# Kernel optimization log

Hardware: AMD Instinct MI355X
Metric: run time of the kernel (lower is better)

## Reference

```python
import jax, jax.numpy as jnp
import numpy as np

N_HEAD = 16
CHUNK_SIZE = 64
TOP_B = 8
LOCAL_WINDOW = 256


def _l2_normalize(x, eps=1e-12):
    # matches torch F.normalize(dim=-1): x / max(||x||, eps)
    n = jnp.sqrt(jnp.sum(x * x, axis=-1, keepdims=True))
    return x / jnp.maximum(n, eps)


def setup_inputs() -> dict:
    key = jax.random.key(0)
    ks = jax.random.split(key, 9)
    B, T, C = 2, 2048, 1024
    s = lambda fan_in: 1.0 / np.sqrt(fan_in)
    return {
        "x": jax.random.normal(ks[0], (B, T, C), jnp.float32),
        "Wqkv": jax.random.normal(ks[1], (C, 3 * C), jnp.float32) * s(C),
        "bqkv": jax.random.normal(ks[2], (3 * C,), jnp.float32) * 0.02,
        "Wproj": jax.random.normal(ks[3], (C, C), jnp.float32) * s(C),
        "bproj": jax.random.normal(ks[4], (C,), jnp.float32) * 0.02,
        "Wrouter": jax.random.normal(ks[5], (C, 32), jnp.float32) * s(C),
        "brouter": jax.random.normal(ks[6], (32,), jnp.float32) * 0.02,
        "Wq_rt": jax.random.normal(ks[7], (C, 32), jnp.float32) * s(C),
        "bq_rt": jax.random.normal(ks[8], (32,), jnp.float32) * 0.02,
    }


def reference(x, Wqkv, bqkv, Wproj, bproj, Wrouter, brouter, Wq_rt, bq_rt):
    B, T, C = x.shape
    H = N_HEAD
    D = C // H

    # --- qkv projection ---
    qkv = x @ Wqkv + bqkv                       # [B,T,3C]
    q, k, v = jnp.split(qkv, 3, axis=-1)
    q = q.reshape(B, T, H, D).transpose(0, 2, 1, 3)  # [B,H,T,D]
    k = k.reshape(B, T, H, D).transpose(0, 2, 1, 3)
    v = v.reshape(B, T, H, D).transpose(0, 2, 1, 3)

    # --- routing (T > local_window + chunk_size) ---
    num_chunks = T // CHUNK_SIZE                 # T divisible -> no padding, mask all-True
    chunk_means = x.reshape(B, num_chunks, CHUNK_SIZE, C).mean(axis=2)  # [B,N,C]
    routing_embeds = chunk_means @ Wrouter + brouter                     # [B,N,32]
    q_rt = _l2_normalize(x @ Wq_rt + bq_rt)                              # [B,T,32]
    re_n = _l2_normalize(routing_embeds)
    routing_scores = jnp.einsum('btd,bnd->btn', q_rt, re_n)              # [B,T,N]
    _, chunk_indices = jax.lax.top_k(routing_scores, TOP_B)              # [B,T,top_b]

    # --- dense causal attention (forward path uses is_causal SDPA) ---
    scale = 1.0 / jnp.sqrt(jnp.asarray(D, x.dtype))
    scores = jnp.einsum('bhqd,bhkd->bhqk', q, k) * scale                 # [B,H,T,T]
    causal = jnp.tril(jnp.ones((T, T), dtype=bool))
    scores = jnp.where(causal[None, None], scores, -jnp.inf)
    attn = jax.nn.softmax(scores, axis=-1)
    y = jnp.einsum('bhqk,bhkd->bhqd', attn, v)                           # [B,H,T,D]
    y = y.transpose(0, 2, 1, 3).reshape(B, T, C)
    y = y @ Wproj + bproj

    return y, chunk_indices, routing_scores, routing_embeds
```

## Files before the change

kernel.cpp:

```cpp
#include <hip/hip_runtime.h>
#include <hip/hip_bf16.h>
#include <math.h>

#define B_   2
#define T_   2048
#define C_   1024
#define H_   16
#define D_   64
#define NCH  32
#define RD   32
#define TOPB 8

typedef __attribute__((ext_vector_type(8))) short bf16x8;
typedef __attribute__((ext_vector_type(4))) float f32x4;

static __device__ __forceinline__ unsigned short f2b(float f) {
    return __bfloat16_as_ushort(__float2bfloat16(f));
}

__global__ __launch_bounds__(256) void cast_bf16_kernel(
    const float* __restrict__ in, unsigned short* __restrict__ out, int n8)
{
    const int i = blockIdx.x * blockDim.x + threadIdx.x;
    if (i >= n8) return;
    float4 a = ((const float4*)in)[i * 2];
    float4 b = ((const float4*)in)[i * 2 + 1];
    bf16x8 o;
    o[0] = (short)f2b(a.x); o[1] = (short)f2b(a.y);
    o[2] = (short)f2b(a.z); o[3] = (short)f2b(a.w);
    o[4] = (short)f2b(b.x); o[5] = (short)f2b(b.y);
    o[6] = (short)f2b(b.z); o[7] = (short)f2b(b.w);
    *(bf16x8*)&out[i * 8] = o;
}

__global__ __launch_bounds__(256) void transpose_cast_kernel(
    const float* __restrict__ W, unsigned short* __restrict__ Wt, int K, int N)
{
    __shared__ float t[64][65];
    const int tid = threadIdx.x;
    const int n0 = blockIdx.x * 64, k0 = blockIdx.y * 64;
#pragma unroll
    for (int i = 0; i < 4; i++) {
        const int f = tid + i * 256;
        const int r = f >> 4, c4 = (f & 15) * 4;
        float4 v = *(const float4*)&W[(size_t)(k0 + r) * N + n0 + c4];
        t[r][c4 + 0] = v.x; t[r][c4 + 1] = v.y;
        t[r][c4 + 2] = v.z; t[r][c4 + 3] = v.w;
    }
    __syncthreads();
#pragma unroll
    for (int i = 0; i < 2; i++) {
        const int s = tid + i * 256;
        const int rn = s >> 3, ck8 = (s & 7) * 8;
        bf16x8 o;
#pragma unroll
        for (int j = 0; j < 8; j++) o[j] = (short)f2b(t[ck8 + j][rn]);
        *(bf16x8*)&Wt[(size_t)(n0 + rn) * K + k0 + ck8] = o;
    }
}

template <int MODE>
__global__ __launch_bounds__(256) void gemm_mfma(
    const unsigned short* __restrict__ A, const unsigned short* __restrict__ Bt,
    const float* __restrict__ bias, float* __restrict__ out,
    unsigned short* __restrict__ qp, unsigned short* __restrict__ kp,
    unsigned short* __restrict__ vp, int M, int N, int K)
{
    __shared__ unsigned short As[2][128 * 32];
    __shared__ unsigned short Bs[2][128 * 32];

    const int tid  = threadIdx.x;
    const int lane = tid & 63;
    const int wave = tid >> 6;
    const int lr = lane & 15, lg = lane >> 4;
    const int wm = wave >> 1, wn = wave & 1;
    const int n0 = blockIdx.x * 128, m0 = blockIdx.y * 128;

    const int srow = tid >> 2;
    const int scol = (tid & 3) * 8;
    const unsigned short* ga = A  + (size_t)(m0 + srow) * K + scol;
    const unsigned short* gb = Bt + (size_t)(n0 + srow) * K + scol;
    const int ldst = (tid & 0xC0) * 8;

    f32x4 acc[4][4];
#pragma unroll
    for (int i = 0; i < 4; i++)
#pragma unroll
        for (int j = 0; j < 4; j++) acc[i][j] = (f32x4){0.f, 0.f, 0.f, 0.f};

#define GSTAGE(buf, k0)                                                        \
    _Pragma("unroll")                                                          \
    for (int i = 0; i < 2; i++) {                                              \
        __builtin_amdgcn_global_load_lds(                                      \
            (const __attribute__((address_space(1))) int*)(ga + (k0) + (size_t)i * 64 * K), \
            (__attribute__((address_space(3))) int*)&As[buf][i * 2048 + ldst], 16, 0, 0);   \
        __builtin_amdgcn_global_load_lds(                                      \
            (const __attribute__((address_space(1))) int*)(gb + (k0) + (size_t)i * 64 * K), \
            (__attribute__((address_space(3))) int*)&Bs[buf][i * 2048 + ldst], 16, 0, 0);   \
    }

    const int nt = K >> 5;
    GSTAGE(0, 0);
    __syncthreads();

    int cur = 0;
    for (int t = 0; t < nt; ++t) {
        if (t + 1 < nt) {
            GSTAGE(cur ^ 1, (t + 1) << 5);
        }

        bf16x8 af[4], bfr[4];
#pragma unroll
        for (int mi = 0; mi < 4; mi++)
            af[mi] = *(const bf16x8*)&As[cur][(wm * 64 + mi * 16 + lr) * 32 + lg * 8];
#pragma unroll
        for (int ni = 0; ni < 4; ni++)
            bfr[ni] = *(const bf16x8*)&Bs[cur][(wn * 64 + ni * 16 + lr) * 32 + lg * 8];
#pragma unroll
        for (int mi = 0; mi < 4; mi++)
#pragma unroll
            for (int ni = 0; ni < 4; ni++)
                acc[mi][ni] = __builtin_amdgcn_mfma_f32_16x16x32_bf16(
                    af[mi], bfr[ni], acc[mi][ni], 0, 0, 0);

        __syncthreads();
        cur ^= 1;
    }
#undef GSTAGE

#pragma unroll
    for (int ni = 0; ni < 4; ni++) {
        const int col = n0 + wn * 64 + ni * 16 + lr;
        const float bv = bias[col];
        if (MODE == 0) {
#pragma unroll
            for (int mi = 0; mi < 4; mi++) {
#pragma unroll
                for (int r = 0; r < 4; r++) {
                    const int row = m0 + wm * 64 + mi * 16 + lg * 4 + r;
                    out[(size_t)row * N + col] = acc[mi][ni][r] + bv;
                }
            }
        } else {
            const int which = col >> 10;
            const int c  = col & 1023;
            const int hh = c >> 6;
            const int dd = c & 63;
            unsigned short* dst = (which == 0) ? qp : (which == 1) ? kp : vp;
#pragma unroll
            for (int mi = 0; mi < 4; mi++) {
#pragma unroll
                for (int r = 0; r < 4; r++) {
                    const int row = m0 + wm * 64 + mi * 16 + lg * 4 + r;
                    const int bb = row >> 11, tt = row & 2047;
                    dst[(((size_t)bb * H_ + hh) * T_ + tt) * D_ + dd] =
                        f2b(acc[mi][ni][r] + bv);
                }
            }
        }
    }
}

__global__ void chunk_mean_kernel(const float* __restrict__ x, float* __restrict__ cm)
{
    const int bc = blockIdx.x;
    const int b = bc >> 5, n = bc & 31;
    const int c = blockIdx.y * 256 + threadIdx.x;
    const float* xp = x + ((size_t)b * T_ + n * 64) * C_;
    float s = 0.f;
    for (int i = 0; i < 64; i++) s += xp[(size_t)i * C_ + c];
    cm[(size_t)bc * C_ + c] = s * (1.0f / 64.0f);
}

__global__ void rowgemm32(const float* __restrict__ A, const float* __restrict__ W,
                          const float* __restrict__ bias, float* __restrict__ dst,
                          int M, int normalize)
{
    const int row  = blockIdx.x * 8 + (threadIdx.x >> 5);
    const int lane = threadIdx.x & 31;
    if (row >= M) return;
    const float* a = A + (size_t)row * C_;
    float acc = 0.f;
    for (int k = 0; k < C_; k += 4) {
        float4 a4 = *(const float4*)&a[k];
        acc += a4.x * W[(k + 0) * RD + lane];
        acc += a4.y * W[(k + 1) * RD + lane];
        acc += a4.z * W[(k + 2) * RD + lane];
        acc += a4.w * W[(k + 3) * RD + lane];
    }
    acc += bias[lane];
    if (normalize) {
        float ss = acc * acc;
#pragma unroll
        for (int off = 16; off >= 1; off >>= 1) ss += __shfl_xor(ss, off, 32);
        acc = acc / fmaxf(sqrtf(ss), 1e-12f);
    }
    dst[(size_t)row * RD + lane] = acc;
}

__global__ void l2norm_rows(const float* __restrict__ src, float* __restrict__ dst, int M)
{
    const int row  = blockIdx.x * 8 + (threadIdx.x >> 5);
    const int lane = threadIdx.x & 31;
    if (row >= M) return;
    float v = src[(size_t)row * RD + lane];
    float ss = v * v;
#pragma unroll
    for (int off = 16; off >= 1; off >>= 1) ss += __shfl_xor(ss, off, 32);
    dst[(size_t)row * RD + lane] = v / fmaxf(sqrtf(ss), 1e-12f);
}

__global__ __launch_bounds__(256) void qrt_kernel(
    const float* __restrict__ x, const float* __restrict__ W,
    const float* __restrict__ bias, float* __restrict__ dst)
{
    __shared__ float part[8][4][32];
    const int r0 = blockIdx.x * 4;
    const int g = threadIdx.x >> 5;
    const int n = threadIdx.x & 31;

    const float* w  = W + (size_t)(g * 128) * RD + n;
    const float* a0 = x + (size_t)(r0 + 0) * C_ + g * 128;
    const float* a1 = x + (size_t)(r0 + 1) * C_ + g * 128;
    const float* a2 = x + (size_t)(r0 + 2) * C_ + g * 128;
    const float* a3 = x + (size_t)(r0 + 3) * C_ + g * 128;

    float acc0 = 0.f, acc1 = 0.f, acc2 = 0.f, acc3 = 0.f;
#pragma unroll 8
    for (int i = 0; i < 128; i += 4) {
        const float w0 = w[(i + 0) * RD];
        const float w1 = w[(i + 1) * RD];
        const float w2 = w[(i + 2) * RD];
        const float w3 = w[(i + 3) * RD];
        float4 x0 = *(const float4*)&a0[i];
        float4 x1 = *(const float4*)&a1[i];
        float4 x2 = *(const float4*)&a2[i];
        float4 x3 = *(const float4*)&a3[i];
        acc0 += x0.x * w0; acc0 += x0.y * w1; acc0 += x0.z * w2; acc0 += x0.w * w3;
        acc1 += x1.x * w0; acc1 += x1.y * w1; acc1 += x1.z * w2; acc1 += x1.w * w3;
        acc2 += x2.x * w0; acc2 += x2.y * w1; acc2 += x2.z * w2; acc2 += x2.w * w3;
        acc3 += x3.x * w0; acc3 += x3.y * w1; acc3 += x3.z * w2; acc3 += x3.w * w3;
    }
    part[g][0][n] = acc0;
    part[g][1][n] = acc1;
    part[g][2][n] = acc2;
    part[g][3][n] = acc3;
    __syncthreads();

    if (g < 4) {
        float s = part[0][g][n];
#pragma unroll
        for (int gg = 1; gg < 8; gg++) s += part[gg][g][n];
        s += bias[n];
        float ss = s * s;
#pragma unroll
        for (int off = 16; off >= 1; off >>= 1) ss += __shfl_xor(ss, off, 32);
        dst[(size_t)(r0 + g) * RD + n] = s / fmaxf(sqrtf(ss), 1e-12f);
    }
}

__global__ void scores_topk(const float* __restrict__ qrt, const float* __restrict__ ren,
                            float* __restrict__ sc_out, float* __restrict__ idx_out)
{
    const int row = blockIdx.x * 64 + threadIdx.x;
    if (row >= B_ * T_) return;
    const int b = row / T_;
    float q[RD];
#pragma unroll
    for (int i = 0; i < RD; i++) q[i] = qrt[(size_t)row * RD + i];
    const float* rb = ren + (size_t)b * NCH * RD;
    float s[NCH];
#pragma unroll 4
    for (int n = 0; n < NCH; n++) {
        float acc = 0.f;
#pragma unroll
        for (int i = 0; i < RD; i++) acc += q[i] * rb[n * RD + i];
        s[n] = acc;
        sc_out[(size_t)row * NCH + n] = acc;
    }
    unsigned mask = 0;
    for (int t = 0; t < TOPB; t++) {
        float best = -INFINITY;
        int bi = 0;
#pragma unroll
        for (int n = 0; n < NCH; n++) {
            const bool ok = !((mask >> n) & 1u) && (s[n] > best);
            if (ok) { best = s[n]; bi = n; }
        }
        mask |= (1u << bi);
        idx_out[(size_t)row * TOPB + t] = (float)bi;
    }
}

#define LSTR 68
#define SCALE2 0.18033688f

__global__ __launch_bounds__(256) void attn_mfma(
    const unsigned short* __restrict__ qg, const unsigned short* __restrict__ kg,
    const unsigned short* __restrict__ vg, unsigned short* __restrict__ y)
{
    const int bid = blockIdx.x;
    const int xcd = bid & 7;
    const int j   = bid >> 3;
    const int h   = xcd + 8 * (j & 1);
    const int b   = (j >> 1) & 1;
    const int qt  = 31 - (j >> 2);

    const int tid  = threadIdx.x;
    const int wave = tid >> 6;
    const int lane = tid & 63;
    const int lg = lane >> 4;
    const int lr = lane & 15;

    __shared__ short Ks[2][64][LSTR];
    __shared__ short Vt[2][64][LSTR];

    const size_t base = ((size_t)(b * H_ + h) * T_) * D_;

    bf16x8 qf0, qf1;
    {
        const short* qp = (const short*)qg + base + (size_t)(qt * 64 + wave * 16 + lr) * D_;
        qf0 = *(const bf16x8*)&qp[lg * 8];
        qf1 = *(const bf16x8*)&qp[32 + lg * 8];
    }

    const int srr = tid >> 2;
    const int sc0 = (tid & 3) * 16;
    const int vrp = tid & 31;
    const int vcg = tid >> 5;
    const int kv0   = 2 * vrp;
    const int vslot = ((kv0 >> 5) << 5) + (((kv0 >> 2) & 3) << 3) +
                      (((kv0 >> 4) & 1) << 2) + (kv0 & 3);

    bf16x8 kreg0, kreg1, vreg0, vreg1;

    float m_run = -INFINITY, l_run = 0.f;
    f32x4 oacc[4];
#pragma unroll
    for (int r = 0; r < 4; r++) oacc[r] = (f32x4){0.f, 0.f, 0.f, 0.f};
    const int qrow_g = qt * 64 + wave * 16 + lr;

    {
        const short* kp = (const short*)kg + base + (size_t)srr * D_ + sc0;
        kreg0 = *(const bf16x8*)kp;
        kreg1 = *(const bf16x8*)(kp + 8);
        const short* vp = (const short*)vg + base + (size_t)kv0 * D_ + vcg * 8;
        vreg0 = *(const bf16x8*)vp;
        vreg1 = *(const bf16x8*)(vp + D_);
    }
    {
        *(bf16x8*)&Ks[0][srr][sc0]     = kreg0;
        *(bf16x8*)&Ks[0][srr][sc0 + 8] = kreg1;
#pragma unroll
        for (int jj = 0; jj < 8; jj++) {
            const unsigned int dw = ((unsigned int)(unsigned short)vreg0[jj]) |
                                    (((unsigned int)(unsigned short)vreg1[jj]) << 16);
            *(unsigned int*)&Vt[0][vcg * 8 + jj][vslot] = dw;
        }
    }
    if (qt >= 1) {
        const short* kp = (const short*)kg + base + (size_t)(64 + srr) * D_ + sc0;
        kreg0 = *(const bf16x8*)kp;
        kreg1 = *(const bf16x8*)(kp + 8);
        const short* vp = (const short*)vg + base + (size_t)(64 + kv0) * D_ + vcg * 8;
        vreg0 = *(const bf16x8*)vp;
        vreg1 = *(const bf16x8*)(vp + D_);
    }
    __syncthreads();

    for (int kt = 0; kt <= qt; ++kt) {
        const int cur = kt & 1;

        if (kt < qt) {
            *(bf16x8*)&Ks[cur ^ 1][srr][sc0]     = kreg0;
            *(bf16x8*)&Ks[cur ^ 1][srr][sc0 + 8] = kreg1;
#pragma unroll
            for (int jj = 0; jj < 8; jj++) {
                const unsigned int dw = ((unsigned int)(unsigned short)vreg0[jj]) |
                                        (((unsigned int)(unsigned short)vreg1[jj]) << 16);
                *(unsigned int*)&Vt[cur ^ 1][vcg * 8 + jj][vslot] = dw;
            }
        }
        if (kt + 2 <= qt) {
            const short* kp = (const short*)kg + base + (size_t)((kt + 2) * 64 + srr) * D_ + sc0;
            kreg0 = *(const bf16x8*)kp;
            kreg1 = *(const bf16x8*)(kp + 8);
            const short* vp = (const short*)vg + base + (size_t)((kt + 2) * 64 + kv0) * D_ + vcg * 8;
            vreg0 = *(const bf16x8*)vp;
            vreg1 = *(const bf16x8*)(vp + D_);
        }

        f32x4 s[4];
        __builtin_amdgcn_s_setprio(1);
#pragma unroll
        for (int cb = 0; cb < 4; cb++) {
            bf16x8 kf0 = *(const bf16x8*)&Ks[cur][cb * 16 + lr][lg * 8];
            bf16x8 kf1 = *(const bf16x8*)&Ks[cur][cb * 16 + lr][32 + lg * 8];
            f32x4 acc = (f32x4){0.f, 0.f, 0.f, 0.f};
            acc = __builtin_amdgcn_mfma_f32_16x16x32_bf16(kf0, qf0, acc, 0, 0, 0);
            acc = __builtin_amdgcn_mfma_f32_16x16x32_bf16(kf1, qf1, acc, 0, 0, 0);
            s[cb] = acc;
        }
        __builtin_amdgcn_s_setprio(0);

        if (kt == qt) {
#pragma unroll
            for (int cb = 0; cb < 4; cb++) {
#pragma unroll
                for (int r = 0; r < 4; r++) {
                    float sv = s[cb][r] * SCALE2;
                    if (kt * 64 + cb * 16 + lg * 4 + r > qrow_g) sv = -INFINITY;
                    s[cb][r] = sv;
                }
            }
        } else {
#pragma unroll
            for (int cb = 0; cb < 4; cb++)
#pragma unroll
                for (int r = 0; r < 4; r++) s[cb][r] *= SCALE2;
        }

        float rm = -INFINITY;
#pragma unroll
        for (int cb = 0; cb < 4; cb++)
#pragma unroll
            for (int r = 0; r < 4; r++) rm = fmaxf(rm, s[cb][r]);
        rm = fmaxf(rm, __shfl_xor(rm, 16));
        rm = fmaxf(rm, __shfl_xor(rm, 32));

        if (!__all(rm <= m_run + 8.0f)) {
            const float mnew = fmaxf(m_run, rm);
            const float fsc  = exp2f(m_run - mnew);
            m_run = mnew;
            l_run *= fsc;
            float fr[4];
#pragma unroll
            for (int r = 0; r < 4; r++) fr[r] = __shfl(fsc, lg * 4 + r);
#pragma unroll
            for (int db = 0; db < 4; db++)
#pragma unroll
                for (int r = 0; r < 4; r++) oacc[db][r] *= fr[r];
        }

        float p[4][4];
        float rs = 0.f;
#pragma unroll
        for (int cb = 0; cb < 4; cb++)
#pragma unroll
            for (int r = 0; r < 4; r++) {
                const float pv = exp2f(s[cb][r] - m_run);
                p[cb][r] = pv;
                rs += pv;
            }
        rs += __shfl_xor(rs, 16);
        rs += __shfl_xor(rs, 32);
        l_run += rs;

        bf16x8 pf0, pf1;
#pragma unroll
        for (int r = 0; r < 4; r++) {
            pf0[r]     = (short)f2b(p[0][r]);
            pf0[4 + r] = (short)f2b(p[1][r]);
            pf1[r]     = (short)f2b(p[2][r]);
            pf1[4 + r] = (short)f2b(p[3][r]);
        }

        __builtin_amdgcn_s_setprio(1);
#pragma unroll
        for (int db = 0; db < 4; db++) {
            bf16x8 vf0 = *(const bf16x8*)&Vt[cur][db * 16 + lr][lg * 8];
            bf16x8 vf1 = *(const bf16x8*)&Vt[cur][db * 16 + lr][32 + lg * 8];
            oacc[db] = __builtin_amdgcn_mfma_f32_16x16x32_bf16(pf0, vf0, oacc[db], 0, 0, 0);
            oacc[db] = __builtin_amdgcn_mfma_f32_16x16x32_bf16(pf1, vf1, oacc[db], 0, 0, 0);
        }
        __builtin_amdgcn_s_setprio(0);

        __syncthreads();
    }

#pragma unroll
    for (int r = 0; r < 4; r++) {
        const float lrow = __shfl(l_run, lg * 4 + r);
        const float inv = 1.0f / lrow;
        const int trow = qt * 64 + wave * 16 + lg * 4 + r;
        unsigned short* yp = y + (size_t)(b * T_ + trow) * C_ + h * D_;
#pragma unroll
        for (int db = 0; db < 4; db++)
            yp[db * 16 + lr] = f2b(oacc[db][r] * inv);
    }
}

extern "C" void kernel_launch(void* const* d_in, const int* in_sizes, int n_in,
                              void* d_out, int out_size, void* d_ws, size_t ws_size,
                              hipStream_t stream)
{
    const float* x       = (const float*)d_in[0];
    const float* Wqkv    = (const float*)d_in[1];
    const float* bqkv    = (const float*)d_in[2];
    const float* Wproj   = (const float*)d_in[3];
    const float* bproj   = (const float*)d_in[4];
    const float* Wrouter = (const float*)d_in[5];
    const float* brouter = (const float*)d_in[6];
    const float* Wq_rt   = (const float*)d_in[7];
    const float* bq_rt   = (const float*)d_in[8];

    float* out = (float*)d_out;
    char*  ws  = (char*)d_ws;

    const size_t MT  = (size_t)B_ * T_;
    const size_t QKV = MT * C_;

    unsigned short* xb   = (unsigned short*)ws;
    unsigned short* Wqt  = xb  + QKV;
    unsigned short* Wpt  = Wqt + (size_t)3 * C_ * C_;
    unsigned short* q    = Wpt + (size_t)C_ * C_;
    unsigned short* k    = q + QKV;
    unsigned short* v    = k + QKV;
    unsigned short* yab  = v + QKV;
    float* cm   = (float*)(yab + QKV);
    float* qrt  = cm  + (size_t)B_ * NCH * C_;
    float* ren  = qrt + MT * RD;

    float* y_out   = out;
    float* idx_out = out + QKV;
    float* sc_out  = idx_out + MT * TOPB;
    float* emb_out = sc_out + MT * NCH;

    cast_bf16_kernel<<<(int)(QKV / 8 / 256), 256, 0, stream>>>(x, xb, (int)(QKV / 8));
    transpose_cast_kernel<<<dim3(3 * C_ / 64, C_ / 64), 256, 0, stream>>>(Wqkv, Wqt, C_, 3 * C_);
    transpose_cast_kernel<<<dim3(C_ / 64, C_ / 64), 256, 0, stream>>>(Wproj, Wpt, C_, C_);

    gemm_mfma<1><<<dim3(3 * C_ / 128, MT / 128), 256, 0, stream>>>(
        xb, Wqt, bqkv, nullptr, q, k, v, (int)MT, 3 * C_, C_);

    chunk_mean_kernel<<<dim3(B_ * NCH, 4), 256, 0, stream>>>(x, cm);
    rowgemm32<<<(B_ * NCH + 7) / 8, 256, 0, stream>>>(cm, Wrouter, brouter, emb_out, B_ * NCH, 0);
    l2norm_rows<<<(B_ * NCH + 7) / 8, 256, 0, stream>>>(emb_out, ren, B_ * NCH);
    qrt_kernel<<<(int)(MT / 4), 256, 0, stream>>>(x, Wq_rt, bq_rt, qrt);
    scores_topk<<<(int)(MT / 64), 64, 0, stream>>>(qrt, ren, sc_out, idx_out);

    attn_mfma<<<dim3(1024), 256, 0, stream>>>(q, k, v, yab);

    gemm_mfma<0><<<dim3(C_ / 128, MT / 128), 256, 0, stream>>>(
        yab, Wpt, bproj, y_out, nullptr, nullptr, nullptr, (int)MT, C_, C_);
}
```

Baseline: 209.5 us.

## Replace QKV GEMM with 256x256-tile, triple-buffered, LDS-swizzled MFMA kernel

Adds a dedicated QKV projection kernel that uses 256x256 output tiles with 512 threads, a three-stage global_load_lds pipeline driven by explicit vmcnt waits, an XOR-swizzled LDS layout to cut bank conflicts, block-index swizzling for L2 locality, and setprio around the MFMA loop. The larger tile raises data reuse per loaded byte and the deeper pipeline hides load latency. The output projection is split into its own non-templated f32-output kernel. The trade-off is only 192 blocks on a chip with 256 CUs, so part of the GPU sits idle. The wider tiles also use more registers per thread.

```diff
diff --git a/kernel.cpp b/kernel.cpp
--- a/kernel.cpp
+++ b/kernel.cpp
@@ -59,12 +59,123 @@
     }
 }
 
-template <int MODE>
-__global__ __launch_bounds__(256) void gemm_mfma(
+__global__ __launch_bounds__(512, 1) void gemm_qkv_256(
     const unsigned short* __restrict__ A, const unsigned short* __restrict__ Bt,
-    const float* __restrict__ bias, float* __restrict__ out,
+    const float* __restrict__ bias,
     unsigned short* __restrict__ qp, unsigned short* __restrict__ kp,
     unsigned short* __restrict__ vp, int M, int N, int K)
+{
+    __shared__ unsigned short lds[3][2][8192];
+
+    const int tid  = threadIdx.x;
+    const int wid  = tid >> 6;
+    const int lane = tid & 63;
+    const int lr = lane & 15, lg = lane >> 4;
+    const int wm = wid >> 2, wn = wid & 3;
+
+    const int bid = blockIdx.x;
+    const int swz = (bid & 7) * 24 + (bid >> 3);
+    const int m0 = (swz & 15) << 8;
+    const int n0 = (swz >> 4) << 8;
+
+    const int srow = tid >> 2;
+    const int sswz = (((srow & 3) ^ ((srow >> 2) & 3)) << 4);
+    const int skel = (((tid & 3) << 4) ^ sswz) >> 1;
+    const unsigned short* gA0 = A  + (size_t)(m0 + srow) * K + skel;
+    const unsigned short* gA1 = A  + (size_t)(m0 + srow + 128) * K + skel;
+    const unsigned short* gB0 = Bt + (size_t)(n0 + srow) * K + skel;
+    const unsigned short* gB1 = Bt + (size_t)(n0 + srow + 128) * K + skel;
+    const int lb0 = (wid * 64) * 8;
+    const int lb1 = (wid * 64 + 512) * 8;
+
+#define QSTAGE(sl, kofs)                                                          \
+    __builtin_amdgcn_global_load_lds(                                             \
+        (const __attribute__((address_space(1))) int*)(gA0 + (kofs)),             \
+        (__attribute__((address_space(3))) int*)&lds[sl][0][lb0], 16, 0, 0);      \
+    __builtin_amdgcn_global_load_lds(                                             \
+        (const __attribute__((address_space(1))) int*)(gA1 + (kofs)),             \
+        (__attribute__((address_space(3))) int*)&lds[sl][0][lb1], 16, 0, 0);      \
+    __builtin_amdgcn_global_load_lds(                                             \
+        (const __attribute__((address_space(1))) int*)(gB0 + (kofs)),             \
+        (__attribute__((address_space(3))) int*)&lds[sl][1][lb0], 16, 0, 0);      \
+    __builtin_amdgcn_global_load_lds(                                             \
+        (const __attribute__((address_space(1))) int*)(gB1 + (kofs)),             \
+        (__attribute__((address_space(3))) int*)&lds[sl][1][lb1], 16, 0, 0);
+
+    const int rswz = (((lr & 3) ^ ((lr >> 2) & 3)) << 4);
+    const int acol = (((lg << 4) ^ rswz) >> 1);
+
+    f32x4 acc[8][4];
+#pragma unroll
+    for (int i = 0; i < 8; i++)
+#pragma unroll
+        for (int j = 0; j < 4; j++) acc[i][j] = (f32x4){0.f, 0.f, 0.f, 0.f};
+
+    const int nt = K >> 5;
+
+    QSTAGE(0, 0)
+    QSTAGE(1, 32)
+    asm volatile("s_waitcnt vmcnt(4)" ::: "memory");
+    __builtin_amdgcn_s_barrier();
+
+    int cur = 0;
+    for (int t = 0; t < nt; ++t) {
+        int s2 = cur + 2; if (s2 >= 3) s2 -= 3;
+        if (t + 2 < nt) { QSTAGE(s2, (t + 2) << 5) }
+
+        const unsigned short* sA = &lds[cur][0][0];
+        const unsigned short* sB = &lds[cur][1][0];
+
+        bf16x8 bfr[4];
+#pragma unroll
+        for (int ni = 0; ni < 4; ni++)
+            bfr[ni] = *(const bf16x8*)&sB[(wn * 64 + ni * 16 + lr) * 32 + acol];
+
+        __builtin_amdgcn_s_setprio(1);
+#pragma unroll
+        for (int mi = 0; mi < 8; mi++) {
+            bf16x8 af = *(const bf16x8*)&sA[(wm * 128 + mi * 16 + lr) * 32 + acol];
+#pragma unroll
+            for (int ni = 0; ni < 4; ni++)
+                acc[mi][ni] = __builtin_amdgcn_mfma_f32_16x16x32_bf16(
+                    af, bfr[ni], acc[mi][ni], 0, 0, 0);
+        }
+        __builtin_amdgcn_s_setprio(0);
+
+        if (t + 1 < nt) {
+            if (t + 2 < nt) { asm volatile("s_waitcnt vmcnt(4)" ::: "memory"); }
+            else            { asm volatile("s_waitcnt vmcnt(0)" ::: "memory"); }
+            __builtin_amdgcn_s_barrier();
+        }
+        cur += 1; if (cur == 3) cur = 0;
+    }
+#undef QSTAGE
+
+#pragma unroll
+    for (int ni = 0; ni < 4; ni++) {
+        const int col = n0 + wn * 64 + ni * 16 + lr;
+        const float bv = bias[col];
+        const int which = col >> 10;
+        const int c  = col & 1023;
+        const int hh = c >> 6;
+        const int dd = c & 63;
+        unsigned short* dst = (which == 0) ? qp : (which == 1) ? kp : vp;
+#pragma unroll
+        for (int mi = 0; mi < 8; mi++) {
+#pragma unroll
+            for (int r = 0; r < 4; r++) {
+                const int row = m0 + wm * 128 + mi * 16 + lg * 4 + r;
+                const int bb = row >> 11, tt = row & 2047;
+                dst[(((size_t)bb * H_ + hh) * T_ + tt) * D_ + dd] =
+                    f2b(acc[mi][ni][r] + bv);
+            }
+        }
+    }
+}
+
+__global__ __launch_bounds__(256) void gemm_mfma_f32out(
+    const unsigned short* __restrict__ A, const unsigned short* __restrict__ Bt,
+    const float* __restrict__ bias, float* __restrict__ out, int M, int N, int K)
 {
     __shared__ unsigned short As[2][128 * 32];
     __shared__ unsigned short Bs[2][128 * 32];
@@ -105,9 +216,7 @@
 
     int cur = 0;
     for (int t = 0; t < nt; ++t) {
-        if (t + 1 < nt) {
-            GSTAGE(cur ^ 1, (t + 1) << 5);
-        }
+        if (t + 1 < nt) { GSTAGE(cur ^ 1, (t + 1) << 5); }
 
         bf16x8 af[4], bfr[4];
 #pragma unroll
@@ -132,30 +241,12 @@
     for (int ni = 0; ni < 4; ni++) {
         const int col = n0 + wn * 64 + ni * 16 + lr;
         const float bv = bias[col];
-        if (MODE == 0) {
-#pragma unroll
-            for (int mi = 0; mi < 4; mi++) {
-#pragma unroll
-                for (int r = 0; r < 4; r++) {
-                    const int row = m0 + wm * 64 + mi * 16 + lg * 4 + r;
-                    out[(size_t)row * N + col] = acc[mi][ni][r] + bv;
-                }
-            }
-        } else {
-            const int which = col >> 10;
-            const int c  = col & 1023;
-            const int hh = c >> 6;
-            const int dd = c & 63;
-            unsigned short* dst = (which == 0) ? qp : (which == 1) ? kp : vp;
-#pragma unroll
-            for (int mi = 0; mi < 4; mi++) {
-#pragma unroll
-                for (int r = 0; r < 4; r++) {
-                    const int row = m0 + wm * 64 + mi * 16 + lg * 4 + r;
-                    const int bb = row >> 11, tt = row & 2047;
-                    dst[(((size_t)bb * H_ + hh) * T_ + tt) * D_ + dd] =
-                        f2b(acc[mi][ni][r] + bv);
-                }
+#pragma unroll
+        for (int mi = 0; mi < 4; mi++) {
+#pragma unroll
+            for (int r = 0; r < 4; r++) {
+                const int row = m0 + wm * 64 + mi * 16 + lg * 4 + r;
+                out[(size_t)row * N + col] = acc[mi][ni][r] + bv;
             }
         }
     }
@@ -530,8 +621,8 @@
     transpose_cast_kernel<<<dim3(3 * C_ / 64, C_ / 64), 256, 0, stream>>>(Wqkv, Wqt, C_, 3 * C_);
     transpose_cast_kernel<<<dim3(C_ / 64, C_ / 64), 256, 0, stream>>>(Wproj, Wpt, C_, C_);
 
-    gemm_mfma<1><<<dim3(3 * C_ / 128, MT / 128), 256, 0, stream>>>(
-        xb, Wqt, bqkv, nullptr, q, k, v, (int)MT, 3 * C_, C_);
+    gemm_qkv_256<<<dim3(192), 512, 0, stream>>>(
+        xb, Wqt, bqkv, q, k, v, (int)MT, 3 * C_, C_);
 
     chunk_mean_kernel<<<dim3(B_ * NCH, 4), 256, 0, stream>>>(x, cm);
     rowgemm32<<<(B_ * NCH + 7) / 8, 256, 0, stream>>>(cm, Wrouter, brouter, emb_out, B_ * NCH, 0);
@@ -541,6 +632,6 @@
 
     attn_mfma<<<dim3(1024), 256, 0, stream>>>(q, k, v, yab);
 
-    gemm_mfma<0><<<dim3(C_ / 128, MT / 128), 256, 0, stream>>>(
-        yab, Wpt, bproj, y_out, nullptr, nullptr, nullptr, (int)MT, C_, C_);
-}
+    gemm_mfma_f32out<<<dim3(C_ / 128, MT / 128), 256, 0, stream>>>(
+        yab, Wpt, bproj, y_out, (int)MT, C_, C_);
+}
```

Result: faster. 197.9 us (-5.5%).
